# Kernel optimization log

Measured on AMD Instinct MI355X. Metric: run time of the kernel, lower is better.

Reference implementation:

```python
import jax, jax.numpy as jnp
import numpy as np

N_E = 1024
E_DIM = 256
BETA = 0.25
PERSISTENCE = 0.1
B, T = 16, 1024


def setup_inputs() -> dict:
    key = jax.random.key(0)
    k1, k2 = jax.random.split(key)
    z = jax.random.normal(k1, (B, T, E_DIM), dtype=jnp.float32)
    # nn.Embedding(1+n_e, e_dim) init uniform(-1/n_e, 1/n_e)
    emb_weight = jax.random.uniform(k2, (N_E + 1, E_DIM), dtype=jnp.float32,
                                    minval=-1.0 / N_E, maxval=1.0 / N_E)
    return {"z": z, "emb_weight": emb_weight}


def _loss_contrast(z, ind, book):
    # z: (B,T,e), ind: (B,T) int, book: (n_e+1, e)
    z_q = book[ind]                                   # (B,T,e)
    loss_indices = jnp.sum((z - z_q) ** 2, axis=-1)   # (B,T)
    # ||z - book||^2 expanded to avoid the (B,T,n_e+1,e) intermediate
    z_sq = jnp.sum(z * z, axis=-1)                    # (B,T)
    b_sq = jnp.sum(book * book, axis=-1)              # (n_e+1,)
    cross = jnp.einsum('bte,ne->btn', z, book)        # (B,T,n_e+1)
    loss_all = z_sq[..., None] + b_sq[None, None, :] - 2.0 * cross
    lc = jnp.maximum(loss_indices[..., None] - loss_all + 1e-6 / N_E, 0.0)
    return jnp.mean(lc)


def _forward(z, emb_weight):
    zf = z.reshape(-1, E_DIM)
    d = (jnp.sum(zf * zf, axis=1, keepdims=True)
         + jnp.sum(emb_weight * emb_weight, axis=1)
         - 2.0 * (zf @ emb_weight.T)).reshape(B, T, N_E + 1)

    ind0 = jnp.clip(jnp.argmin(d[:, 0, :], axis=1), 0, N_E - 1)  # (B,)

    def step(carry, d_t):
        ind, coe = carry                              # (B,) int, (B,) f32
        d_here = jnp.take_along_axis(d_t, ind[:, None], axis=1)[:, 0]
        ind_next = jnp.minimum(ind + 1, N_E - 1)
        d_next = jnp.take_along_axis(d_t, ind_next[:, None], axis=1)[:, 0]
        stay = d_here <= d_next - coe
        ind_new = jnp.where(stay, ind, ind_next)
        coe_new = jnp.where(stay, coe + PERSISTENCE / N_E, 0.0)
        return (ind_new, coe_new), ind_new

    coe0 = jnp.zeros((B,), jnp.float32)
    _, inds = jax.lax.scan(step, (ind0, coe0), jnp.swapaxes(d[:, 1:, :], 0, 1))
    encoding_indices = jnp.concatenate([ind0[None, :], inds], axis=0).T  # (B,T)

    book_sg = jax.lax.stop_gradient(emb_weight)  # torch uses .data/.detach() everywhere
    z_q_raw = book_sg[encoding_indices]
    z_q = z + jax.lax.stop_gradient(z_q_raw - z)  # straight-through

    # non-legacy: beta * L(z, sg(book)) + L(sg(z), sg(book))
    loss = (BETA * _loss_contrast(z, encoding_indices, book_sg)
            + _loss_contrast(jax.lax.stop_gradient(z), encoding_indices, book_sg))

    v = jnp.max(encoding_indices) - jnp.min(encoding_indices)
    return z_q, loss, encoding_indices, v


def reference(z, emb_weight):
    return _forward(z, emb_weight)
```

## Files before the change

kernel.cpp:

```cpp
#include <hip/hip_runtime.h>

#define N_E   1024
#define EDIM  256
#define BB    16
#define TT    1024
#define NROW  (BB*TT)
#define NCOL  1025
#define NPAD  1152
#define PERS  (0.1f/1024.0f)
#define EPSC  (1e-6f/1024.0f)

#define OUT_LOSS 4194304
#define OUT_IDX  4194305
#define OUT_V    4210689

#define WS_ZB   0ull
#define WS_BBF  8388608ull
#define WS_BSQ  8978432ull
#define WS_E    8983552ull
#define WS_IND  84481024ull
#define WS_PART 84546560ull

typedef __attribute__((ext_vector_type(8))) short short8;
typedef __attribute__((ext_vector_type(4))) float floatx4;

__device__ __forceinline__ unsigned short f2bf(float f) {
    unsigned int u = __float_as_uint(f);
    u = (u + 0x7fffu + ((u >> 16) & 1u)) >> 16;
    return (unsigned short)u;
}

__global__ __launch_bounds__(256) void k0_prep(const float* __restrict__ z,
                                               const float* __restrict__ book,
                                               unsigned short* __restrict__ zb,
                                               unsigned short* __restrict__ bb,
                                               float* __restrict__ bsq) {
    int bx = blockIdx.x, tid = threadIdx.x;
    if (bx < 4096) {
        float4 v = ((const float4*)z)[bx * 256 + tid];
        size_t o = ((size_t)bx * 256 + tid) * 4;
        zb[o + 0] = f2bf(v.x); zb[o + 1] = f2bf(v.y);
        zb[o + 2] = f2bf(v.z); zb[o + 3] = f2bf(v.w);
    } else {
        int row = bx - 4096;
        float v = (row < NCOL) ? book[(size_t)row * EDIM + tid] : 0.0f;
        bb[(size_t)row * EDIM + tid] = f2bf(v);
        __shared__ float sd[256];
        sd[tid] = v * v;
        __syncthreads();
        for (int s = 128; s > 0; s >>= 1) { if (tid < s) sd[tid] += sd[tid + s]; __syncthreads(); }
        if (tid == 0) bsq[row] = sd[0];
    }
}

__global__ __launch_bounds__(256) void k1_gemm(const unsigned short* __restrict__ zb,
                                               const unsigned short* __restrict__ bb,
                                               const float* __restrict__ bsq,
                                               float* __restrict__ e) {
    int tid = threadIdx.x;
    int lane = tid & 63, w = tid >> 6;
    int mBase = blockIdx.x * 128 + (w >> 1) * 64;
    int nBase = blockIdx.y * 128 + (w & 1) * 64;
    int r = lane & 15, q = lane >> 4;

    floatx4 acc[4][4];
    #pragma unroll
    for (int i = 0; i < 4; i++)
        #pragma unroll
        for (int j = 0; j < 4; j++) acc[i][j] = (floatx4){0.f, 0.f, 0.f, 0.f};

    const short8* A = (const short8*)zb;
    const short8* Bm = (const short8*)bb;

    #pragma unroll
    for (int ks = 0; ks < 8; ks++) {
        int k8 = ks * 4 + q;
        short8 a[4], b[4];
        #pragma unroll
        for (int i = 0; i < 4; i++) a[i] = A[(size_t)(mBase + i * 16 + r) * 32 + k8];
        #pragma unroll
        for (int j = 0; j < 4; j++) b[j] = Bm[(size_t)(nBase + j * 16 + r) * 32 + k8];
        #pragma unroll
        for (int i = 0; i < 4; i++)
            #pragma unroll
            for (int j = 0; j < 4; j++)
                acc[i][j] = __builtin_amdgcn_mfma_f32_16x16x32_bf16(a[i], b[j], acc[i][j], 0, 0, 0);
    }

    float bsql[4];
    #pragma unroll
    for (int j = 0; j < 4; j++) bsql[j] = bsq[nBase + j * 16 + r];

    #pragma unroll
    for (int i = 0; i < 4; i++)
        #pragma unroll
        for (int rr = 0; rr < 4; rr++) {
            int m = mBase + i * 16 + q * 4 + rr;
            float* erow = e + (size_t)m * NPAD;
            #pragma unroll
            for (int j = 0; j < 4; j++)
                erow[nBase + j * 16 + r] = fmaf(-2.0f, acc[i][j][rr], bsql[j]);
        }
}

__global__ __launch_bounds__(256, 1) void k2_scan(const float* __restrict__ z,
                                                  const float* __restrict__ book,
                                                  const float* __restrict__ bsq,
                                                  const float* __restrict__ e,
                                                  int* __restrict__ wind) {
    int b = blockIdx.x, tid = threadIdx.x;
    int lane = tid & 63, w = tid >> 6;

    const float4* zr = (const float4*)(z + (size_t)b * TT * EDIM);
    float4 zv = zr[lane];
    float s = zv.x * zv.x + zv.y * zv.y + zv.z * zv.z + zv.w * zv.w;
    #pragma unroll
    for (int off = 32; off; off >>= 1) s += __shfl_xor(s, off, 64);
    float zsq = s;

    float best = 3.4e38f; int bidx = 0;
    for (int wi = w; wi < 17; wi += 4) {
        int n = wi * 64 + lane;
        if (n < NCOL) {
            const float4* br = (const float4*)(book + (size_t)n * EDIM);
            float c0 = 0.f, c1 = 0.f, c2 = 0.f, c3 = 0.f;
            #pragma unroll 8
            for (int k = 0; k < 64; k++) {
                float4 bo = br[k]; float4 za = zr[k];
                c0 = fmaf(za.x, bo.x, c0); c1 = fmaf(za.y, bo.y, c1);
                c2 = fmaf(za.z, bo.z, c2); c3 = fmaf(za.w, bo.w, c3);
            }
            float cr = (c0 + c1) + (c2 + c3);
            float d0 = (zsq + bsq[n]) - 2.0f * cr;
            if (d0 < best || (d0 == best && n < bidx)) { best = d0; bidx = n; }
        }
    }
    #pragma unroll
    for (int off = 32; off; off >>= 1) {
        float ob = __shfl_xor(best, off, 64);
        int   oi = __shfl_xor(bidx, off, 64);
        if (ob < best || (ob == best && oi < bidx)) { best = ob; bidx = oi; }
    }
    __shared__ float sb[4]; __shared__ int si[4];
    if (lane == 0) { sb[w] = best; si[w] = bidx; }
    __syncthreads();
    if (w != 0) return;

    best = sb[0]; bidx = si[0];
    for (int i = 1; i < 4; i++) {
        float vv = sb[i]; int ii = si[i];
        if (vv < best || (vv == best && ii < bidx)) { best = vv; bidx = ii; }
    }

    int ind = min(bidx, N_E - 1);
    int kk = 0;
    size_t ibase = (size_t)b * TT;
    if (lane == 0) wind[ibase] = ind;

    const float* eb = e + (size_t)b * TT * NPAD;
    const float QS = 1.0f / PERS;

    float Av[31], Bv[31];
    int   q[31];

    int cb = min(ind, 960);
    {
        #pragma unroll
        for (int j = 0; j < 31; j++) {
            const float* p = eb + (size_t)(1 + j) * NPAD + cb + lane;
            Av[j] = p[0]; Bv[j] = p[1];
        }
        bool cap = (cb + lane == 1023);
        #pragma unroll
        for (int j = 0; j < 31; j++) {
            int qv = (int)((Bv[j] - Av[j]) * QS);
            q[j] = cap ? 0 : qv;
        }
    }

    int t = 1;
    for (int c = 0; c < 33; c++) {
        int cbn = min(ind, 960);
        if (c < 32) {
            #pragma unroll
            for (int j = 0; j < 31; j++) {
                int tn = t + 31 + j; tn = tn < 1024 ? tn : 1023;
                const float* p = eb + (size_t)tn * NPAD + cbn + lane;
                Av[j] = p[0]; Bv[j] = p[1];
            }
        }
        int packed = 0;
        #pragma unroll
        for (int j = 0; j < 31; j++) {
            int rel = ind - cb;
            int qv = __builtin_amdgcn_readlane(q[j], rel);
            bool stay = (kk <= qv);
            int ip1 = ind + 1; ip1 = ip1 < 1023 ? ip1 : 1023;
            ind = stay ? ind : ip1;
            kk  = stay ? kk + 1 : 0;
            packed = (lane == j) ? ind : packed;
        }
        if (lane < 31) wind[ibase + t + lane] = packed;
        if (c < 32) {
            bool cap = (cbn + lane == 1023);
            #pragma unroll
            for (int j = 0; j < 31; j++) {
                int qv = (int)((Bv[j] - Av[j]) * QS);
                q[j] = cap ? 0 : qv;
            }
        }
        cb = cbn;
        t += 31;
    }
}

__global__ __launch_bounds__(256) void k3_loss_zq(const float* __restrict__ e,
                                                  const int* __restrict__ wind,
                                                  const float* __restrict__ book,
                                                  float* __restrict__ part,
                                                  float* __restrict__ out) {
    int rIdx = blockIdx.x, tid = threadIdx.x;
    int ind = wind[rIdx];
    const float* er = e + (size_t)rIdx * NPAD;
    float eind = er[ind];
    float p = 0.0f;
    for (int n = tid; n < NCOL; n += 256) {
        float v = eind - er[n] + EPSC;
        p += v > 0.0f ? v : 0.0f;
    }
    __shared__ float sd[256];
    sd[tid] = p; __syncthreads();
    for (int s = 128; s > 0; s >>= 1) { if (tid < s) sd[tid] += sd[tid + s]; __syncthreads(); }
    if (tid == 0) { part[rIdx] = sd[0]; out[OUT_IDX + rIdx] = (float)ind; }
    out[(size_t)rIdx * 256 + tid] = book[(size_t)ind * EDIM + tid];
}

__global__ __launch_bounds__(256) void k4_final(const float* __restrict__ part,
                                                const int* __restrict__ wind,
                                                float* __restrict__ out) {
    int tid = threadIdx.x;
    float s = 0.0f;
    for (int i = tid; i < NROW; i += 256) s += part[i];
    __shared__ float sd[256];
    sd[tid] = s; __syncthreads();
    for (int st = 128; st > 0; st >>= 1) { if (tid < st) sd[tid] += sd[tid + st]; __syncthreads(); }
    if (tid == 0) {
        int mn = wind[0], mx = wind[TT - 1];
        for (int b = 1; b < BB; b++) {
            mn = min(mn, wind[(size_t)b * TT]);
            mx = max(mx, wind[(size_t)b * TT + TT - 1]);
        }
        out[OUT_LOSS] = 1.25f * sd[0] / ((float)NROW * (float)NCOL);
        out[OUT_V] = (float)(mx - mn);
    }
}

extern "C" void kernel_launch(void* const* d_in, const int* in_sizes, int n_in,
                              void* d_out, int out_size, void* d_ws, size_t ws_size,
                              hipStream_t stream) {
    const float* z    = (const float*)d_in[0];
    const float* book = (const float*)d_in[1];
    char* ws = (char*)d_ws;
    unsigned short* zb = (unsigned short*)(ws + WS_ZB);
    unsigned short* bb = (unsigned short*)(ws + WS_BBF);
    float* bsq  = (float*)(ws + WS_BSQ);
    float* e    = (float*)(ws + WS_E);
    int*   wind = (int*)(ws + WS_IND);
    float* part = (float*)(ws + WS_PART);
    float* out  = (float*)d_out;

    hipLaunchKernelGGL(k0_prep,    dim3(4096 + 1152), dim3(256), 0, stream, z, book, zb, bb, bsq);
    hipLaunchKernelGGL(k1_gemm,    dim3(128, 9),      dim3(256), 0, stream, zb, bb, bsq, e);
    hipLaunchKernelGGL(k2_scan,    dim3(16),          dim3(256), 0, stream, z, book, bsq, e, wind);
    hipLaunchKernelGGL(k3_loss_zq, dim3(16384),       dim3(256), 0, stream, e, wind, book, part, out);
    hipLaunchKernelGGL(k4_final,   dim3(1),           dim3(256), 0, stream, part, wind, out);
}
```

Baseline: 260.3 us.

## Precompute quantized stay thresholds in a parallel pass before the serial scan

Adds a fully parallel kernel that converts each row of the distance matrix into int16 stay thresholds (quantized difference of adjacent columns). The serial 16-block scan then loads only one short per lane per step instead of two floats and no longer does the conversion arithmetic inside its critical loop. The initial argmin is split into its own kernel. This adds a full pass over the 75MB distance matrix, a new 32MB buffer and two extra launches, in exchange for a shorter latency-bound scan.

```diff
diff --git a/kernel.cpp b/kernel.cpp
--- a/kernel.cpp
+++ b/kernel.cpp
@@ -20,6 +20,7 @@
 #define WS_E    8983552ull
 #define WS_IND  84481024ull
 #define WS_PART 84546560ull
+#define WS_Q    84612096ull
 
 typedef __attribute__((ext_vector_type(8))) short short8;
 typedef __attribute__((ext_vector_type(4))) float floatx4;
@@ -103,10 +104,26 @@
         }
 }
 
-__global__ __launch_bounds__(256, 1) void k2_scan(const float* __restrict__ z,
+__global__ __launch_bounds__(256) void k1b_q(const float* __restrict__ e,
+                                             short* __restrict__ q16) {
+    int row = blockIdx.x, tid = threadIdx.x;
+    const float* er = e + (size_t)row * NPAD;
+    short* qr = q16 + (size_t)row * 1024;
+    const float QS = 1.0f / PERS;
+    #pragma unroll
+    for (int i = 0; i < 4; i++) {
+        int c = tid + i * 256;
+        float a = er[c], bv = er[c + 1];
+        float x = (bv - a) * QS;
+        int qv = (x >= 0.0f) ? min((int)x, 1023) : -1;
+        if (c == 1023) qv = 0;
+        qr[c] = (short)qv;
+    }
+}
+
+__global__ __launch_bounds__(256) void k2a_argmin(const float* __restrict__ z,
                                                   const float* __restrict__ book,
                                                   const float* __restrict__ bsq,
-                                                  const float* __restrict__ e,
                                                   int* __restrict__ wind) {
     int b = blockIdx.x, tid = threadIdx.x;
     int lane = tid & 63, w = tid >> 6;
@@ -144,39 +161,30 @@
     __shared__ float sb[4]; __shared__ int si[4];
     if (lane == 0) { sb[w] = best; si[w] = bidx; }
     __syncthreads();
-    if (w != 0) return;
+    if (tid != 0) return;
 
     best = sb[0]; bidx = si[0];
     for (int i = 1; i < 4; i++) {
         float vv = sb[i]; int ii = si[i];
         if (vv < best || (vv == best && ii < bidx)) { best = vv; bidx = ii; }
     }
-
-    int ind = min(bidx, N_E - 1);
+    wind[(size_t)b * TT] = min(bidx, N_E - 1);
+}
+
+__global__ __launch_bounds__(64, 1) void k2b_scan(const short* __restrict__ q16,
+                                                  int* __restrict__ wind) {
+    int b = blockIdx.x, lane = threadIdx.x;
+    size_t ibase = (size_t)b * TT;
+    int ind = wind[ibase];
     int kk = 0;
-    size_t ibase = (size_t)b * TT;
-    if (lane == 0) wind[ibase] = ind;
-
-    const float* eb = e + (size_t)b * TT * NPAD;
-    const float QS = 1.0f / PERS;
-
-    float Av[31], Bv[31];
-    int   q[31];
+
+    const short* qb = q16 + (size_t)b * TT * 1024;
+    int cur[31], nxt[31];
 
     int cb = min(ind, 960);
-    {
-        #pragma unroll
-        for (int j = 0; j < 31; j++) {
-            const float* p = eb + (size_t)(1 + j) * NPAD + cb + lane;
-            Av[j] = p[0]; Bv[j] = p[1];
-        }
-        bool cap = (cb + lane == 1023);
-        #pragma unroll
-        for (int j = 0; j < 31; j++) {
-            int qv = (int)((Bv[j] - Av[j]) * QS);
-            q[j] = cap ? 0 : qv;
-        }
-    }
+    #pragma unroll
+    for (int j = 0; j < 31; j++)
+        cur[j] = qb[(size_t)(1 + j) * 1024 + cb + lane];
 
     int t = 1;
     for (int c = 0; c < 33; c++) {
@@ -185,15 +193,14 @@
             #pragma unroll
             for (int j = 0; j < 31; j++) {
                 int tn = t + 31 + j; tn = tn < 1024 ? tn : 1023;
-                const float* p = eb + (size_t)tn * NPAD + cbn + lane;
-                Av[j] = p[0]; Bv[j] = p[1];
+                nxt[j] = qb[(size_t)tn * 1024 + cbn + lane];
             }
         }
         int packed = 0;
         #pragma unroll
         for (int j = 0; j < 31; j++) {
             int rel = ind - cb;
-            int qv = __builtin_amdgcn_readlane(q[j], rel);
+            int qv = __builtin_amdgcn_readlane(cur[j], rel);
             bool stay = (kk <= qv);
             int ip1 = ind + 1; ip1 = ip1 < 1023 ? ip1 : 1023;
             ind = stay ? ind : ip1;
@@ -201,14 +208,8 @@
             packed = (lane == j) ? ind : packed;
         }
         if (lane < 31) wind[ibase + t + lane] = packed;
-        if (c < 32) {
-            bool cap = (cbn + lane == 1023);
-            #pragma unroll
-            for (int j = 0; j < 31; j++) {
-                int qv = (int)((Bv[j] - Av[j]) * QS);
-                q[j] = cap ? 0 : qv;
-            }
-        }
+        #pragma unroll
+        for (int j = 0; j < 31; j++) cur[j] = nxt[j];
         cb = cbn;
         t += 31;
     }
@@ -267,11 +268,14 @@
     float* e    = (float*)(ws + WS_E);
     int*   wind = (int*)(ws + WS_IND);
     float* part = (float*)(ws + WS_PART);
+    short* q16  = (short*)(ws + WS_Q);
     float* out  = (float*)d_out;
 
     hipLaunchKernelGGL(k0_prep,    dim3(4096 + 1152), dim3(256), 0, stream, z, book, zb, bb, bsq);
     hipLaunchKernelGGL(k1_gemm,    dim3(128, 9),      dim3(256), 0, stream, zb, bb, bsq, e);
-    hipLaunchKernelGGL(k2_scan,    dim3(16),          dim3(256), 0, stream, z, book, bsq, e, wind);
+    hipLaunchKernelGGL(k1b_q,      dim3(NROW),        dim3(256), 0, stream, e, q16);
+    hipLaunchKernelGGL(k2a_argmin, dim3(16),          dim3(256), 0, stream, z, book, bsq, wind);
+    hipLaunchKernelGGL(k2b_scan,   dim3(16),          dim3(64),  0, stream, q16, wind);
     hipLaunchKernelGGL(k3_loss_zq, dim3(16384),       dim3(256), 0, stream, e, wind, book, part, out);
     hipLaunchKernelGGL(k4_final,   dim3(1),           dim3(256), 0, stream, part, wind, out);
 }
```

Measured after the change: 269.2 us. 1.03x slower.
